# Kernel optimization log

Measured on AMD Instinct MI355X. Metric: run time of the kernel, lower is better.

The kernel has to match this reference:

```python
import jax, jax.numpy as jnp
import numpy as np

B, S, D = 4, 2048, 1024

def setup_inputs() -> dict:
    key = jax.random.key(0)
    k1, k2, k3, k4 = jax.random.split(key, 4)
    scale = 1.0 / np.sqrt(D)  # roughly glorot-like magnitude for weights
    return {
        "inputs": jax.random.normal(k1, (B, S, D), dtype=jnp.float32),
        "W_query": jax.random.normal(k2, (D, D), dtype=jnp.float32) * scale,
        "W_key": jax.random.normal(k3, (D, D), dtype=jnp.float32) * scale,
        "W_value": jax.random.normal(k4, (D, D), dtype=jnp.float32) * scale,
    }

def reference(inputs, W_query, W_key, W_value):
    # QKV projections: [B,S,D] @ [D,D]
    q = jnp.einsum('bsd,de->bse', inputs, W_query)
    k = jnp.einsum('bsd,de->bse', inputs, W_key)
    v = jnp.einsum('bsd,de->bse', inputs, W_value)
    # Unscaled attention scores [B,S,S] (source applies no 1/sqrt(d))
    score = jnp.einsum('bqd,bkd->bqk', q, k)
    weights = jax.nn.softmax(score, axis=-1)
    context = jnp.einsum('bqk,bkd->bqd', weights, v)
    return context
```

## Files before the change

### kernel.cpp

```cpp
#include <hip/hip_runtime.h>
#include <math.h>


typedef __bf16 bf16;
typedef _Float16 f16;
typedef __bf16 bf16x8 __attribute__((ext_vector_type(8)));
typedef __bf16 bf16x4 __attribute__((ext_vector_type(4)));
typedef _Float16 f16x4 __attribute__((ext_vector_type(4)));
typedef _Float16 f16x8 __attribute__((ext_vector_type(8)));
typedef float  f32x4  __attribute__((ext_vector_type(4)));

template<typename E> struct vec8_of;
template<> struct vec8_of<bf16> { using type = bf16x8; };
template<> struct vec8_of<f16>  { using type = f16x8; };

__device__ inline f32x4 mfma16(bf16x8 a, bf16x8 b, f32x4 c) {
    return __builtin_amdgcn_mfma_f32_16x16x32_bf16(a, b, c, 0, 0, 0);
}
__device__ inline f32x4 mfma16(f16x8 a, f16x8 b, f32x4 c) {
    return __builtin_amdgcn_mfma_f32_16x16x32_f16(a, b, c, 0, 0, 0);
}

#define AS1 __attribute__((address_space(1)))
#define AS3 __attribute__((address_space(3)))

template<typename E>
__device__ inline void async_load16(const E* g, void* l) {
    __builtin_amdgcn_global_load_lds((const AS1 unsigned int*)g,
                                     (AS3 unsigned int*)l, 16, 0, 0);
}

#define SBAR()  do { __builtin_amdgcn_s_barrier(); __builtin_amdgcn_sched_barrier(0); } while (0)
#define WAITV(n) do { asm volatile("s_waitcnt vmcnt(" #n ")" ::: "memory"); __builtin_amdgcn_sched_barrier(0); } while (0)
#define WAITL() do { asm volatile("s_waitcnt lgkmcnt(0)" ::: "memory"); __builtin_amdgcn_sched_barrier(0); } while (0)

template<int OUT_MODE>
__device__ __forceinline__ void gemm8_body(
    char* __restrict__ smraw,
    const f16* __restrict__ A, const f16* __restrict__ B,
    float* __restrict__ Cf, f16* __restrict__ Ch,
    int K, int lda, int ldb, int ldc,
    long long sA, long long sB, long long sC,
    int bx, int by, int bz)
{
    A += (long long)bz * sA;
    B += (long long)bz * sB;

    const int tid  = threadIdx.x;
    const int lane = tid & 63;
    const int wave = tid >> 6;
    const int quad = lane >> 4;
    const int l16  = lane & 15;
    const int wm   = wave >> 2;
    const int wn   = wave & 3;

    const long long rowA0 = (long long)by * 256;
    const long long colB0 = (long long)bx * 256;

    const int s0 = tid, s1 = 512 + tid;
    const int aRow0 = s0 >> 2, aRow1 = s1 >> 2;
    const int aCol0 = ((s0 & 3) ^ ((s0 >> 4) & 3)) * 8;
    const int aCol1 = ((s1 & 3) ^ ((s1 >> 4) & 3)) * 8;
    const int ci    = s0 >> 2;
    const int bRow0 = (ci >> 5) * 64 + (ci & 31);
    const int bCol  = aCol0;

    const f16* aSrc0 = A + (rowA0 + aRow0) * lda + aCol0;
    const f16* aSrc1 = A + (rowA0 + aRow1) * lda + aCol1;
    const f16* b0Src = B + (colB0 + bRow0) * ldb + bCol;
    const f16* b1Src = b0Src + 32LL * ldb;

    const int dA0 = tid * 16, dA1 = 8192 + tid * 16, dB = tid * 16;

    const int nt = K >> 5;

    auto stageA = [&](int t) {
        char* buf = smraw + ((t & 1) << 15);
        async_load16(aSrc0 + t * 32, buf + dA0);
        async_load16(aSrc1 + t * 32, buf + dA1);
    };
    auto stageB0 = [&](int t) {
        char* buf = smraw + ((t & 1) << 15);
        async_load16(b0Src + t * 32, buf + 16384 + dB);
    };
    auto stageB1 = [&](int t) {
        char* buf = smraw + ((t & 1) << 15);
        async_load16(b1Src + t * 32, buf + 24576 + dB);
    };

    const int lofs = l16 * 64 + ((quad ^ ((l16 >> 2) & 3)) << 4);
    const int aoff = wm * 8192 + lofs;
    const int boff = wn * 2048 + lofs;

    f32x4 acc[8][4];
#pragma unroll
    for (int i = 0; i < 8; i++)
#pragma unroll
        for (int j = 0; j < 4; j++) acc[i][j] = (f32x4){0.f, 0.f, 0.f, 0.f};

    stageA(0); stageB0(0); stageB1(0);
    stageA(1); stageB0(1);
    WAITV(4);
    SBAR();

    for (int t = 0; t < nt; t++) {
        const char* buf = smraw + ((t & 1) << 15);
        f16x8 av[8], bv[2];

#pragma unroll
        for (int i = 0; i < 8; i++) av[i] = *(const f16x8*)(buf + aoff + i * 1024);
#pragma unroll
        for (int j = 0; j < 2; j++) bv[j] = *(const f16x8*)(buf + 16384 + boff + j * 1024);
        if (t + 1 < nt) stageB1(t + 1);
        SBAR();
        WAITL();
        __builtin_amdgcn_s_setprio(1);
#pragma unroll
        for (int i = 0; i < 8; i++) {
            acc[i][0] = mfma16(av[i], bv[0], acc[i][0]);
            acc[i][1] = mfma16(av[i], bv[1], acc[i][1]);
        }
        __builtin_amdgcn_s_setprio(0);
        if (t + 1 < nt) { WAITV(4); } else { WAITV(0); }
        SBAR();

#pragma unroll
        for (int j = 0; j < 2; j++) bv[j] = *(const f16x8*)(buf + 24576 + boff + j * 1024);
        if (t + 2 < nt) { stageA(t + 2); stageB0(t + 2); }
        SBAR();
        WAITL();
        __builtin_amdgcn_s_setprio(1);
#pragma unroll
        for (int i = 0; i < 8; i++) {
            acc[i][2] = mfma16(av[i], bv[0], acc[i][2]);
            acc[i][3] = mfma16(av[i], bv[1], acc[i][3]);
        }
        __builtin_amdgcn_s_setprio(0);
        if (t + 2 < nt) { WAITV(4); }
        else if (t + 1 < nt) { WAITV(1); }
        SBAR();
    }

    if (OUT_MODE == 2) {
        auto tr = (f16(*)[72])smraw;
        const int batch = (int)(rowA0 >> 11);
        const long long rib = rowA0 & 2047;
        const int c  = tid >> 1;
        const int r0 = (tid & 1) << 5;
#pragma unroll
        for (int h = 0; h < 2; h++)
#pragma unroll
            for (int iq = 0; iq < 2; iq++) {
                __syncthreads();
                if (wm == h) {
#pragma unroll
                    for (int i2 = 0; i2 < 4; i2++)
#pragma unroll
                        for (int j = 0; j < 4; j++)
#pragma unroll
                            for (int e = 0; e < 4; e++)
                                tr[wn * 64 + j * 16 + l16][i2 * 16 + quad * 4 + e] =
                                    (f16)acc[iq * 4 + i2][j][e];
                }
                __syncthreads();
                f16* vt = Ch + (long long)batch * 1024 * 2048 +
                          (long long)(colB0 + c) * ldc + rib + h * 128 + iq * 64 + r0;
#pragma unroll
                for (int u = 0; u < 32; u += 8)
                    *(f16x8*)(vt + u) = *(const f16x8*)&tr[c][r0 + u];
            }
        return;
    }

    const long long cOff = (long long)bz * sC +
                           (rowA0 + wm * 128 + quad * 4) * (long long)ldc +
                           colB0 + wn * 64 + l16;
#pragma unroll
    for (int i = 0; i < 8; i++)
#pragma unroll
        for (int e = 0; e < 4; e++) {
            const long long ro = cOff + (long long)(i * 16 + e) * ldc;
            if (OUT_MODE == 0) {
                float* rp = Cf + ro;
#pragma unroll
                for (int j = 0; j < 4; j++) rp[j * 16] = acc[i][j][e];
            } else {
                f16* rp = Ch + ro;
#pragma unroll
                for (int j = 0; j < 4; j++) rp[j * 16] = (f16)acc[i][j][e];
            }
        }
}

__global__ __launch_bounds__(512, 2) void tv8(
    const f16* __restrict__ Xf, const f16* __restrict__ Mt_f,
    const f16* __restrict__ Wvt_f, f16* __restrict__ T, f16* __restrict__ Vt)
{
    extern __shared__ char smraw[];
    if (blockIdx.x < 4)
        gemm8_body<1>(smraw, Xf, Mt_f, nullptr, T, 1024, 1024, 1024, 1024,
                      0, 0, 0, blockIdx.x, blockIdx.y, 0);
    else
        gemm8_body<2>(smraw, Xf, Wvt_f, nullptr, Vt, 1024, 1024, 1024, 2048,
                      0, 0, 0, blockIdx.x - 4, blockIdx.y, 0);
}

template<int OUT_MODE>
__global__ __launch_bounds__(512, 2) void gemm8_k(
    const f16* __restrict__ A, const f16* __restrict__ B,
    float* __restrict__ Cf, f16* __restrict__ Ch,
    int K, int lda, int ldb, int ldc,
    long long sA, long long sB, long long sC)
{
    extern __shared__ char smraw[];
    gemm8_body<OUT_MODE>(smraw, A, B, Cf, Ch, K, lda, ldb, ldc, sA, sB, sC,
                         blockIdx.x, blockIdx.y, blockIdx.z);
}

template<typename E, bool SPLIT, int OUT_MODE, int BK>
__device__ __forceinline__ void gemm_body(
    char* __restrict__ smraw,
    const E* __restrict__ Ahi, const E* __restrict__ Alo,
    const E* __restrict__ Bhi, const E* __restrict__ Blo,
    float* __restrict__ Cf, f16* __restrict__ Ch,
    int K, int lda, int ldb, int ldc,
    long long sA, long long sB, long long sC,
    int bx, int by, int bz)
{
    using vec8 = typename vec8_of<E>::type;
    constexpr int TILE_BYTES = 128 * BK * (int)sizeof(E);
    constexpr int CPW = (TILE_BYTES / 1024) / 4;
    constexpr int SPR = (BK * (int)sizeof(E)) / 16;

    Ahi += (long long)bz * sA;
    Bhi += (long long)bz * sB;
    if (SPLIT) { Alo += (long long)bz * sA; Blo += (long long)bz * sB; }

    const int tid  = threadIdx.x;
    const int lane = tid & 63;
    const int wave = tid >> 6;
    const int quad = lane >> 4;
    const int l16  = lane & 15;
    const int wm   = (wave >> 1) * 64;
    const int wn   = (wave & 1) * 64;

    const long long rowA0 = (long long)by * 128;
    const long long colB0 = (long long)bx * 128;

    auto swz = [](int r) -> int { return (SPR == 8) ? (r & 7) : ((r >> 1) & 3); };

    int ofs[CPW], rr[CPW], cc8[CPW];
#pragma unroll
    for (int u = 0; u < CPW; u++) {
        ofs[u] = (wave * CPW + u) * 1024 + lane * 16;
        const int s = ofs[u] >> 4;
        rr[u]  = s / SPR;
        cc8[u] = (s & (SPR - 1)) ^ swz(rr[u]);
    }

    f32x4 acc[4][4];
#pragma unroll
    for (int i = 0; i < 4; i++)
#pragma unroll
        for (int j = 0; j < 4; j++) acc[i][j] = (f32x4){0.f, 0.f, 0.f, 0.f};

    for (int k0 = 0; k0 < K; k0 += BK) {
#pragma unroll
        for (int u = 0; u < CPW; u++) {
            async_load16(Ahi + (rowA0 + rr[u]) * lda + k0 + cc8[u] * 8, smraw + 0 * TILE_BYTES + ofs[u]);
            async_load16(Bhi + (colB0 + rr[u]) * ldb + k0 + cc8[u] * 8, smraw + 1 * TILE_BYTES + ofs[u]);
            if (SPLIT) {
                async_load16(Alo + (rowA0 + rr[u]) * lda + k0 + cc8[u] * 8, smraw + 2 * TILE_BYTES + ofs[u]);
                async_load16(Blo + (colB0 + rr[u]) * ldb + k0 + cc8[u] * 8, smraw + 3 * TILE_BYTES + ofs[u]);
            }
        }
        __syncthreads();

#pragma unroll
        for (int kh = 0; kh < BK / 32; kh++) {
            const int kc8 = kh * 4 + quad;
            vec8 a_hi[4], b_hi[4], a_lo[4], b_lo[4];
#pragma unroll
            for (int i = 0; i < 4; i++) {
                const int ra = wm + i * 16 + l16;
                const int rb = wn + i * 16 + l16;
                const int oa = ra * (SPR * 16) + ((kc8 ^ swz(ra)) << 4);
                const int ob = rb * (SPR * 16) + ((kc8 ^ swz(rb)) << 4);
                a_hi[i] = *(const vec8*)(smraw + 0 * TILE_BYTES + oa);
                b_hi[i] = *(const vec8*)(smraw + 1 * TILE_BYTES + ob);
                if (SPLIT) {
                    a_lo[i] = *(const vec8*)(smraw + 2 * TILE_BYTES + oa);
                    b_lo[i] = *(const vec8*)(smraw + 3 * TILE_BYTES + ob);
                }
            }
#pragma unroll
            for (int i = 0; i < 4; i++)
#pragma unroll
                for (int j = 0; j < 4; j++) {
                    acc[i][j] = mfma16(a_hi[i], b_hi[j], acc[i][j]);
                    if (SPLIT) {
                        acc[i][j] = mfma16(a_hi[i], b_lo[j], acc[i][j]);
                        acc[i][j] = mfma16(a_lo[i], b_hi[j], acc[i][j]);
                    }
                }
        }
        __syncthreads();
    }

    const long long cOff = (long long)bz * sC +
                           (rowA0 + wm + quad * 4) * (long long)ldc + colB0 + wn + l16;
#pragma unroll
    for (int i = 0; i < 4; i++)
#pragma unroll
        for (int e = 0; e < 4; e++) {
            const long long ro = cOff + (i * 16 + e) * ldc;
            if (OUT_MODE == 0) {
                float* rp = Cf + ro;
#pragma unroll
                for (int j = 0; j < 4; j++) rp[j * 16] = acc[i][j][e];
            } else {
                f16* rp = Ch + ro;
#pragma unroll
                for (int j = 0; j < 4; j++) rp[j * 16] = (f16)acc[i][j][e];
            }
        }
}

template<typename E, bool SPLIT, int OUT_MODE, int BK>
__global__ __launch_bounds__(256) void gemm_bt(
    const E* __restrict__ Ahi, const E* __restrict__ Alo,
    const E* __restrict__ Bhi, const E* __restrict__ Blo,
    float* __restrict__ Cf, f16* __restrict__ Ch,
    int K, int lda, int ldb, int ldc,
    long long sA, long long sB, long long sC)
{
    extern __shared__ char smraw[];
    gemm_body<E, SPLIT, OUT_MODE, BK>(smraw, Ahi, Alo, Bhi, Blo, Cf, Ch,
                                      K, lda, ldb, ldc, sA, sB, sC,
                                      blockIdx.x, blockIdx.y, blockIdx.z);
}

__global__ __launch_bounds__(256) void prep_all(
    const float4* __restrict__ X, f16* __restrict__ Xf,
    const float* __restrict__ Wq, const float* __restrict__ Wk, const float* __restrict__ Wv,
    bf16* __restrict__ Wq_h, bf16* __restrict__ Wq_l,
    bf16* __restrict__ Wk_h, bf16* __restrict__ Wk_l,
    f16* __restrict__ Wvt_f)
{
    int b = blockIdx.x;
    if (b < 8192) {
        long long i = (long long)b * 256 + threadIdx.x;
        float4 v = X[i];
        f16x4 fv = {(f16)v.x, (f16)v.y, (f16)v.z, (f16)v.w};
        *(f16x4*)(Xf + 4 * i) = fv;
    } else if (b < 10240) {
        const int b2 = b - 8192;
        const float4* W = (const float4*)(b2 < 1024 ? Wq : Wk);
        bf16* hh = b2 < 1024 ? Wq_h : Wk_h;
        bf16* ll = b2 < 1024 ? Wq_l : Wk_l;
        long long i = (long long)(b2 & 1023) * 256 + threadIdx.x;
        float4 v = W[i];
        bf16 a0 = (bf16)v.x, a1 = (bf16)v.y, a2 = (bf16)v.z, a3 = (bf16)v.w;
        bf16x4 hv = {a0, a1, a2, a3};
        bf16x4 lv = {(bf16)(v.x - (float)a0), (bf16)(v.y - (float)a1),
                     (bf16)(v.z - (float)a2), (bf16)(v.w - (float)a3)};
        *(bf16x4*)(hh + 4 * i) = hv;
        *(bf16x4*)(ll + 4 * i) = lv;
    } else {
        const int b3 = b - 10240;
        __shared__ float t[32][33];
        const int bx = (b3 & 31) * 32, by = (b3 >> 5) * 32;
        const int tx = threadIdx.x & 31, ty = threadIdx.x >> 5;
#pragma unroll
        for (int i = 0; i < 32; i += 8)
            t[ty + i][tx] = Wv[(long long)(by + ty + i) * 1024 + bx + tx];
        __syncthreads();
#pragma unroll
        for (int i = 0; i < 32; i += 8) {
            long long o = (long long)(bx + ty + i) * 1024 + by + tx;
            Wvt_f[o] = (f16)t[tx][ty + i];
        }
    }
}

__global__ __launch_bounds__(256) void softmax_f16(const float* __restrict__ S,
                                                   f16* __restrict__ P, int n)
{
    const long long row = blockIdx.x;
    const float4* p = (const float4*)(S + row * (long long)n);
    f16* q = P + row * (long long)n;
    const int tid = threadIdx.x;
    const int wv = tid >> 6, lane = tid & 63;

    float4 va = p[tid], vb = p[tid + 256];
    float v[8] = {va.x, va.y, va.z, va.w, vb.x, vb.y, vb.z, vb.w};
    float m = -3.4e38f;
#pragma unroll
    for (int i = 0; i < 8; i++) m = fmaxf(m, v[i]);
#pragma unroll
    for (int off = 32; off > 0; off >>= 1) m = fmaxf(m, __shfl_xor(m, off, 64));

    __shared__ float red[4];
    if (lane == 0) red[wv] = m;
    __syncthreads();
    m = fmaxf(fmaxf(red[0], red[1]), fmaxf(red[2], red[3]));

    float s = 0.f;
#pragma unroll
    for (int i = 0; i < 8; i++) { v[i] = __expf(v[i] - m); s += v[i]; }
#pragma unroll
    for (int off = 32; off > 0; off >>= 1) s += __shfl_xor(s, off, 64);
    __syncthreads();
    if (lane == 0) red[wv] = s;
    __syncthreads();
    s = red[0] + red[1] + red[2] + red[3];

    const float inv = 1.0f / s;
    f16x4 o0 = {(f16)(v[0] * inv), (f16)(v[1] * inv), (f16)(v[2] * inv), (f16)(v[3] * inv)};
    f16x4 o1 = {(f16)(v[4] * inv), (f16)(v[5] * inv), (f16)(v[6] * inv), (f16)(v[7] * inv)};
    *(f16x4*)(q + tid * 4) = o0;
    *(f16x4*)(q + 1024 + tid * 4) = o1;
}

extern "C" void kernel_launch(void* const* d_in, const int* in_sizes, int n_in,
                              void* d_out, int out_size, void* d_ws, size_t ws_size,
                              hipStream_t stream) {
    const float* X  = (const float*)d_in[0];
    const float* Wq = (const float*)d_in[1];
    const float* Wk = (const float*)d_in[2];
    const float* Wv = (const float*)d_in[3];
    float* out = (float*)d_out;

    char* w = (char*)d_ws;
    const long long MB = 1024LL * 1024;
    f16*  Xf    = (f16*) (w + 0 * MB);
    bf16* Wq_h  = (bf16*)(w + 16 * MB);
    bf16* Wq_l  = (bf16*)(w + 18 * MB);
    bf16* Wk_h  = (bf16*)(w + 20 * MB);
    bf16* Wk_l  = (bf16*)(w + 22 * MB);
    f16*  Wvt_f = (f16*) (w + 24 * MB);
    f16*  Mt_f  = (f16*) (w + 26 * MB);
    f16*  T     = (f16*) (w + 28 * MB);
    f16*  Vt    = (f16*) (w + 44 * MB);
    float* Sc   = (float*)(w + 60 * MB);
    f16*  P     = (f16*) (w + 124 * MB);

    dim3 blk(256);

    prep_all<<<dim3(11264), blk, 0, stream>>>(
        (const float4*)X, Xf, Wq, Wk, Wv, Wq_h, Wq_l, Wk_h, Wk_l, Wvt_f);

    gemm_bt<bf16, true, 1, 32><<<dim3(8, 8, 1), blk, 32768, stream>>>(
        Wk_h, Wk_l, Wq_h, Wq_l, nullptr, Mt_f,
        1024, 1024, 1024, 1024, 0, 0, 0);

    tv8<<<dim3(8, 32), dim3(512), 65536, stream>>>(Xf, Mt_f, Wvt_f, T, Vt);

    gemm8_k<0><<<dim3(8, 8, 4), dim3(512), 65536, stream>>>(
        T, Xf, Sc, nullptr, 1024, 1024, 1024, 2048,
        2048LL * 1024, 2048LL * 1024, 2048LL * 2048);

    softmax_f16<<<dim3(4 * 2048), blk, 0, stream>>>(Sc, P, 2048);

    gemm8_k<0><<<dim3(4, 8, 4), dim3(512), 65536, stream>>>(
        P, Vt, out, nullptr, 2048, 2048, 2048, 1024,
        2048LL * 2048, 1024LL * 2048, 2048LL * 1024);
}
```

Measured before the change: 313.2 us.

## Add XCD-aware block swizzle, new LDS swizzle, and half-height tiles for PV GEMM

Block indices are remapped so that neighbouring tiles land on the same XCD, which is meant to improve L2 reuse across the chiplets. The LDS staging layout and the read swizzle are rewritten to a 128-byte row pattern to cut bank conflicts. The GEMM body is templated on tile height, and the final P·V GEMM uses 128-row tiles with twice as many blocks and less LDS. That gives better occupancy and CU coverage for the small grid, at the cost of less A/B reuse per block.

After: 273.3 us. -12.7%, faster.

```diff
diff --git a/kernel.cpp b/kernel.cpp
--- a/kernel.cpp
+++ b/kernel.cpp
@@ -34,7 +34,14 @@
 #define WAITV(n) do { asm volatile("s_waitcnt vmcnt(" #n ")" ::: "memory"); __builtin_amdgcn_sched_barrier(0); } while (0)
 #define WAITL() do { asm volatile("s_waitcnt lgkmcnt(0)" ::: "memory"); __builtin_amdgcn_sched_barrier(0); } while (0)
 
-template<int OUT_MODE>
+__device__ inline void xcd_swz(int nwg, int gx, int& bx, int& by) {
+    const int flat = by * gx + bx;
+    const int s = (flat & 7) * (nwg >> 3) + (flat >> 3);
+    bx = s % gx;
+    by = s / gx;
+}
+
+template<int OUT_MODE, int BMQ>
 __device__ __forceinline__ void gemm8_body(
     char* __restrict__ smraw,
     const f16* __restrict__ A, const f16* __restrict__ B,
@@ -43,6 +50,10 @@
     long long sA, long long sB, long long sC,
     int bx, int by, int bz)
 {
+    constexpr int B0OFF = BMQ * 8192;
+    constexpr int B1OFF = B0OFF + 8192;
+    constexpr int BUFSZ = B0OFF + 16384;
+
     A += (long long)bz * sA;
     B += (long long)bz * sB;
 
@@ -54,105 +65,105 @@
     const int wm   = wave >> 2;
     const int wn   = wave & 3;
 
-    const long long rowA0 = (long long)by * 256;
+    const long long rowA0 = (long long)by * (BMQ * 128);
     const long long colB0 = (long long)bx * 256;
 
-    const int s0 = tid, s1 = 512 + tid;
-    const int aRow0 = s0 >> 2, aRow1 = s1 >> 2;
-    const int aCol0 = ((s0 & 3) ^ ((s0 >> 4) & 3)) * 8;
-    const int aCol1 = ((s1 & 3) ^ ((s1 >> 4) & 3)) * 8;
-    const int ci    = s0 >> 2;
-    const int bRow0 = (ci >> 5) * 64 + (ci & 31);
-    const int bCol  = aCol0;
+    const int line0 = tid >> 3;
+    const int slog  = (tid & 7) ^ (line0 & 7);
+    const int aRow0 = line0 * 2 + (slog >> 2);
+    const int aCol0 = (slog & 3) * 8;
+    const int bRow  = ((aRow0 >> 5) << 6) + (aRow0 & 31);
 
     const f16* aSrc0 = A + (rowA0 + aRow0) * lda + aCol0;
-    const f16* aSrc1 = A + (rowA0 + aRow1) * lda + aCol1;
-    const f16* b0Src = B + (colB0 + bRow0) * ldb + bCol;
+    const f16* aSrc1 = A + (rowA0 + 128 + aRow0) * lda + aCol0;
+    const f16* b0Src = B + (colB0 + bRow) * ldb + aCol0;
     const f16* b1Src = b0Src + 32LL * ldb;
 
-    const int dA0 = tid * 16, dA1 = 8192 + tid * 16, dB = tid * 16;
+    const int dA0 = tid * 16, dA1 = 8192 + tid * 16;
 
     const int nt = K >> 5;
 
     auto stageA = [&](int t) {
-        char* buf = smraw + ((t & 1) << 15);
+        char* buf = smraw + (t & 1) * BUFSZ;
         async_load16(aSrc0 + t * 32, buf + dA0);
-        async_load16(aSrc1 + t * 32, buf + dA1);
+        if (BMQ == 2) async_load16(aSrc1 + t * 32, buf + dA1);
     };
     auto stageB0 = [&](int t) {
-        char* buf = smraw + ((t & 1) << 15);
-        async_load16(b0Src + t * 32, buf + 16384 + dB);
+        char* buf = smraw + (t & 1) * BUFSZ;
+        async_load16(b0Src + t * 32, buf + B0OFF + dA0);
     };
     auto stageB1 = [&](int t) {
-        char* buf = smraw + ((t & 1) << 15);
-        async_load16(b1Src + t * 32, buf + 24576 + dB);
+        char* buf = smraw + (t & 1) * BUFSZ;
+        async_load16(b1Src + t * 32, buf + B1OFF + dA0);
     };
 
-    const int lofs = l16 * 64 + ((quad ^ ((l16 >> 2) & 3)) << 4);
-    const int aoff = wm * 8192 + lofs;
+    const int h    = l16 >> 1;
+    const int lofs = h * 128 + ((((l16 & 1) * 4 + quad) ^ h) << 4);
+    const int aoff = wm * (BMQ * 4096) + lofs;
     const int boff = wn * 2048 + lofs;
 
-    f32x4 acc[8][4];
-#pragma unroll
-    for (int i = 0; i < 8; i++)
+    f32x4 acc[4 * BMQ][4];
+#pragma unroll
+    for (int i = 0; i < 4 * BMQ; i++)
 #pragma unroll
         for (int j = 0; j < 4; j++) acc[i][j] = (f32x4){0.f, 0.f, 0.f, 0.f};
 
     stageA(0); stageB0(0); stageB1(0);
     stageA(1); stageB0(1);
-    WAITV(4);
+    if constexpr (BMQ == 2) WAITV(4); else WAITV(3);
     SBAR();
 
     for (int t = 0; t < nt; t++) {
-        const char* buf = smraw + ((t & 1) << 15);
-        f16x8 av[8], bv[2];
-
-#pragma unroll
-        for (int i = 0; i < 8; i++) av[i] = *(const f16x8*)(buf + aoff + i * 1024);
-#pragma unroll
-        for (int j = 0; j < 2; j++) bv[j] = *(const f16x8*)(buf + 16384 + boff + j * 1024);
+        const char* buf = smraw + (t & 1) * BUFSZ;
+        f16x8 av[4 * BMQ], bv[2];
+
+#pragma unroll
+        for (int i = 0; i < 4 * BMQ; i++) av[i] = *(const f16x8*)(buf + aoff + i * 1024);
+#pragma unroll
+        for (int j = 0; j < 2; j++) bv[j] = *(const f16x8*)(buf + B0OFF + boff + j * 1024);
         if (t + 1 < nt) stageB1(t + 1);
         SBAR();
         WAITL();
         __builtin_amdgcn_s_setprio(1);
 #pragma unroll
-        for (int i = 0; i < 8; i++) {
+        for (int i = 0; i < 4 * BMQ; i++) {
             acc[i][0] = mfma16(av[i], bv[0], acc[i][0]);
             acc[i][1] = mfma16(av[i], bv[1], acc[i][1]);
         }
         __builtin_amdgcn_s_setprio(0);
-        if (t + 1 < nt) { WAITV(4); } else { WAITV(0); }
+        if (t + 1 < nt) { if constexpr (BMQ == 2) WAITV(4); else WAITV(3); }
+        else WAITV(0);
         SBAR();
 
 #pragma unroll
-        for (int j = 0; j < 2; j++) bv[j] = *(const f16x8*)(buf + 24576 + boff + j * 1024);
+        for (int j = 0; j < 2; j++) bv[j] = *(const f16x8*)(buf + B1OFF + boff + j * 1024);
         if (t + 2 < nt) { stageA(t + 2); stageB0(t + 2); }
         SBAR();
         WAITL();
         __builtin_amdgcn_s_setprio(1);
 #pragma unroll
-        for (int i = 0; i < 8; i++) {
+        for (int i = 0; i < 4 * BMQ; i++) {
             acc[i][2] = mfma16(av[i], bv[0], acc[i][2]);
             acc[i][3] = mfma16(av[i], bv[1], acc[i][3]);
         }
         __builtin_amdgcn_s_setprio(0);
-        if (t + 2 < nt) { WAITV(4); }
-        else if (t + 1 < nt) { WAITV(1); }
+        if (t + 2 < nt) { if constexpr (BMQ == 2) WAITV(4); else WAITV(3); }
+        else if (t + 1 < nt) WAITV(1);
         SBAR();
     }
 
-    if (OUT_MODE == 2) {
+    if constexpr (OUT_MODE == 2) {
         auto tr = (f16(*)[72])smraw;
         const int batch = (int)(rowA0 >> 11);
         const long long rib = rowA0 & 2047;
         const int c  = tid >> 1;
         const int r0 = (tid & 1) << 5;
 #pragma unroll
-        for (int h = 0; h < 2; h++)
+        for (int h2 = 0; h2 < 2; h2++)
 #pragma unroll
             for (int iq = 0; iq < 2; iq++) {
                 __syncthreads();
-                if (wm == h) {
+                if (wm == h2) {
 #pragma unroll
                     for (int i2 = 0; i2 < 4; i2++)
 #pragma unroll
@@ -164,7 +175,7 @@
                 }
                 __syncthreads();
                 f16* vt = Ch + (long long)batch * 1024 * 2048 +
-                          (long long)(colB0 + c) * ldc + rib + h * 128 + iq * 64 + r0;
+                          (long long)(colB0 + c) * ldc + rib + h2 * 128 + iq * 64 + r0;
 #pragma unroll
                 for (int u = 0; u < 32; u += 8)
                     *(f16x8*)(vt + u) = *(const f16x8*)&tr[c][r0 + u];
@@ -173,10 +184,10 @@
     }
 
     const long long cOff = (long long)bz * sC +
-                           (rowA0 + wm * 128 + quad * 4) * (long long)ldc +
+                           (rowA0 + wm * (BMQ * 64) + quad * 4) * (long long)ldc +
                            colB0 + wn * 64 + l16;
 #pragma unroll
-    for (int i = 0; i < 8; i++)
+    for (int i = 0; i < 4 * BMQ; i++)
 #pragma unroll
         for (int e = 0; e < 4; e++) {
             const long long ro = cOff + (long long)(i * 16 + e) * ldc;
@@ -197,15 +208,17 @@
     const f16* __restrict__ Wvt_f, f16* __restrict__ T, f16* __restrict__ Vt)
 {
     extern __shared__ char smraw[];
-    if (blockIdx.x < 4)
-        gemm8_body<1>(smraw, Xf, Mt_f, nullptr, T, 1024, 1024, 1024, 1024,
-                      0, 0, 0, blockIdx.x, blockIdx.y, 0);
+    int bx = blockIdx.x, by = blockIdx.y;
+    xcd_swz(256, 8, bx, by);
+    if (bx < 4)
+        gemm8_body<1, 2>(smraw, Xf, Mt_f, nullptr, T, 1024, 1024, 1024, 1024,
+                         0, 0, 0, bx, by, 0);
     else
-        gemm8_body<2>(smraw, Xf, Wvt_f, nullptr, Vt, 1024, 1024, 1024, 2048,
-                      0, 0, 0, blockIdx.x - 4, blockIdx.y, 0);
-}
-
-template<int OUT_MODE>
+        gemm8_body<2, 2>(smraw, Xf, Wvt_f, nullptr, Vt, 1024, 1024, 1024, 2048,
+                         0, 0, 0, bx - 4, by, 0);
+}
+
+template<int OUT_MODE, int BMQ>
 __global__ __launch_bounds__(512, 2) void gemm8_k(
     const f16* __restrict__ A, const f16* __restrict__ B,
     float* __restrict__ Cf, f16* __restrict__ Ch,
@@ -213,8 +226,10 @@
     long long sA, long long sB, long long sC)
 {
     extern __shared__ char smraw[];
-    gemm8_body<OUT_MODE>(smraw, A, B, Cf, Ch, K, lda, ldb, ldc, sA, sB, sC,
-                         blockIdx.x, blockIdx.y, blockIdx.z);
+    int bx = blockIdx.x, by = blockIdx.y;
+    xcd_swz(gridDim.x * gridDim.y, gridDim.x, bx, by);
+    gemm8_body<OUT_MODE, BMQ>(smraw, A, B, Cf, Ch, K, lda, ldb, ldc, sA, sB, sC,
+                              bx, by, blockIdx.z);
 }
 
 template<typename E, bool SPLIT, int OUT_MODE, int BK>
@@ -456,13 +471,13 @@
 
     tv8<<<dim3(8, 32), dim3(512), 65536, stream>>>(Xf, Mt_f, Wvt_f, T, Vt);
 
-    gemm8_k<0><<<dim3(8, 8, 4), dim3(512), 65536, stream>>>(
+    gemm8_k<0, 2><<<dim3(8, 8, 4), dim3(512), 65536, stream>>>(
         T, Xf, Sc, nullptr, 1024, 1024, 1024, 2048,
         2048LL * 1024, 2048LL * 1024, 2048LL * 2048);
 
     softmax_f16<<<dim3(4 * 2048), blk, 0, stream>>>(Sc, P, 2048);
 
-    gemm8_k<0><<<dim3(4, 8, 4), dim3(512), 65536, stream>>>(
+    gemm8_k<0, 1><<<dim3(4, 16, 4), dim3(512), 49152, stream>>>(
         P, Vt, out, nullptr, 2048, 2048, 2048, 1024,
         2048LL * 2048, 1024LL * 2048, 2048LL * 1024);
 }
```
